# Optimization experiments

Measured on AMD Instinct MI355X. Metric: run time of the kernel, lower is better.

Reference implementation:

```python
import jax, jax.numpy as jnp
import numpy as np

B, H, C = 1, 4, 32
D = H * C          # 128
S, L = 128, 256
EPS = 1e-5


def _axial_layer_norm(x, gamma, beta):
    # normalize over channel axis (axis=1) of [B, D, S, L]
    mu = jnp.mean(x, axis=1, keepdims=True)
    var = jnp.var(x, axis=1, keepdims=True)
    xn = (x - mu) * jax.lax.rsqrt(var + EPS)
    return xn * gamma[None, :, None, None] + beta[None, :, None, None]


def setup_inputs() -> dict:
    key = jax.random.key(0)
    ks = jax.random.split(key, 5)
    x = jax.random.normal(ks[0], (B, D, S, L), dtype=jnp.float32)
    w_row = jax.random.normal(ks[1], (3 * D, D), dtype=jnp.float32) * 0.02
    b_row = jax.random.normal(ks[2], (3 * D,), dtype=jnp.float32) * 0.02
    w_col = jax.random.normal(ks[3], (3 * D, D), dtype=jnp.float32) * 0.02
    b_col = jax.random.normal(ks[4], (3 * D,), dtype=jnp.float32) * 0.02
    return {
        "x": x,
        "w_row": w_row, "b_row": b_row,
        "w_col": w_col, "b_col": b_col,
        "gamma1": jnp.ones((D,), jnp.float32), "beta1": jnp.zeros((D,), jnp.float32),
        "gamma2": jnp.ones((D,), jnp.float32), "beta2": jnp.zeros((D,), jnp.float32),
    }


def _qkv(x, w, b):
    # 1x1 conv == channel matmul: [3D, D] x [B, D, S, L] -> [B, 3D, S, L]
    qkv = jnp.einsum('od,bdsl->bosl', w, x) + b[None, :, None, None]
    q, k, v = jnp.split(qkv, 3, axis=1)
    rs = lambda t: t.reshape(t.shape[0], H, C, S, L)
    return rs(q), rs(k), rs(v)


def reference(x, w_row, b_row, w_col, b_col, gamma1, beta1, gamma2, beta2):
    # --- row attention (attend along L within each row s) ---
    q, k, v = _qkv(x, w_row, b_row)
    row_attn = jnp.einsum('bhcsi,bhcsj->bhsij', q, k)   # [B,H,S,L,L], no 1/sqrt(d) scaling (as in source)
    row_attn = jax.nn.softmax(row_attn, axis=-1)
    row_out = jnp.einsum('bhsij,bhdsj->bhdsi', row_attn, v).reshape(x.shape[0], D, S, L)
    out = _axial_layer_norm(x + row_out, gamma1, beta1)

    # --- column attention (attend along S within each column l) ---
    q, k, v = _qkv(out, w_col, b_col)
    col_attn = jnp.einsum('bhcil,bhcjl->bhijl', q, k)   # [B,H,S,S,L]
    col_attn = jax.nn.softmax(col_attn, axis=-2)
    col_out = jnp.einsum('bhijl,bhdjl->bhdil', col_attn, v).reshape(x.shape[0], D, S, L)
    out = _axial_layer_norm(out + col_out, gamma2, beta2)
    return out
```

## Files before the change

kernel.cpp:

```cpp
#include <hip/hip_runtime.h>
#include <hip/hip_bf16.h>

#define SL     32768
#define EPS_LN 1e-5f

typedef unsigned short u16;
typedef __attribute__((ext_vector_type(8))) short bf16x8;
typedef __attribute__((ext_vector_type(4))) float f32x4;

#define MFMA16(a, b, c) __builtin_amdgcn_mfma_f32_16x16x32_bf16((a), (b), (c), 0, 0, 0)

__device__ inline u16 f2bf(float f) {
    __hip_bfloat16 h = __float2bfloat16(f);
    return *reinterpret_cast<u16*>(&h);
}
__device__ inline float bf2f(u16 u) {
    unsigned v = ((unsigned)u) << 16;
    float f;
    __builtin_memcpy(&f, &v, 4);
    return f;
}
__device__ inline uint4 pack8(float4 a, float4 b) {
    union { uint4 v; u16 u[8]; } U;
    U.u[0] = f2bf(a.x); U.u[1] = f2bf(a.y); U.u[2] = f2bf(a.z); U.u[3] = f2bf(a.w);
    U.u[4] = f2bf(b.x); U.u[5] = f2bf(b.y); U.u[6] = f2bf(b.z); U.u[7] = f2bf(b.w);
    return U.v;
}

__global__ __launch_bounds__(256) void wcast_kernel(const float* __restrict__ wr,
                                                    const float* __restrict__ wc,
                                                    u16* __restrict__ wrb,
                                                    u16* __restrict__ wcb) {
    const int i = blockIdx.x * 256 + threadIdx.x;
    const int NW = 384 * 128 / 8;
    const float* src = (i < NW) ? wr : wc;
    u16* dst = (i < NW) ? wrb : wcb;
    const int j = (i < NW) ? i : i - NW;
    float4 a = ((const float4*)src)[j * 2];
    float4 b = ((const float4*)src)[j * 2 + 1];
    ((uint4*)dst)[j] = pack8(a, b);
}

__global__ __launch_bounds__(512) void qkv_mfma(const float* __restrict__ in,
                                                const u16* __restrict__ wb,
                                                const float* __restrict__ bq,
                                                u16* __restrict__ qT,
                                                u16* __restrict__ kT,
                                                u16* __restrict__ vb) {
    __shared__ u16 xT[64][136];
    __shared__ float bs[384];
    const int n0 = blockIdx.x * 64;
    const int t = threadIdx.x;
    const int lane = t & 63, wv = t >> 6, lo = lane & 15, hi = lane >> 4;

    if (t < 384) bs[t] = bq[t];

    #pragma unroll
    for (int itr = 0; itr < 2; ++itr) {
        const int u = t + itr * 512;
        const int d = u & 127, noct = u >> 7;
        const float* src = in + (size_t)d * SL + n0 + noct * 8;
        float4 f0 = *(const float4*)src;
        float4 f1 = *(const float4*)(src + 4);
        xT[noct * 8 + 0][d] = f2bf(f0.x);
        xT[noct * 8 + 1][d] = f2bf(f0.y);
        xT[noct * 8 + 2][d] = f2bf(f0.z);
        xT[noct * 8 + 3][d] = f2bf(f0.w);
        xT[noct * 8 + 4][d] = f2bf(f1.x);
        xT[noct * 8 + 5][d] = f2bf(f1.y);
        xT[noct * 8 + 6][d] = f2bf(f1.z);
        xT[noct * 8 + 7][d] = f2bf(f1.w);
    }
    __syncthreads();

    bf16x8 af[3][4];
    #pragma unroll
    for (int om = 0; om < 3; ++om)
        #pragma unroll
        for (int ks = 0; ks < 4; ++ks)
            af[om][ks] = *(const bf16x8*)(wb + (size_t)(wv * 48 + om * 16 + lo) * 128
                                             + hi * 8 + ks * 32);

    #pragma unroll
    for (int nt = 0; nt < 4; ++nt) {
        const int n = n0 + nt * 16 + lo;
        bf16x8 bfr[4];
        #pragma unroll
        for (int ks = 0; ks < 4; ++ks)
            bfr[ks] = *(const bf16x8*)&xT[nt * 16 + lo][hi * 8 + ks * 32];
        #pragma unroll
        for (int om = 0; om < 3; ++om) {
            const int obase = wv * 48 + om * 16;
            f32x4 acc = {0.f, 0.f, 0.f, 0.f};
            #pragma unroll
            for (int ks = 0; ks < 4; ++ks)
                acc = MFMA16(af[om][ks], bfr[ks], acc);
            if (obase < 256) {
                u16* tbuf = (obase < 128) ? qT : kT;
                const int ob = obase & 127;
                const int h = ob >> 5;
                const int cb = (ob & 31) + hi * 4;
                ushort4 o4;
                o4.x = f2bf(acc[0] + bs[obase + hi * 4 + 0]);
                o4.y = f2bf(acc[1] + bs[obase + hi * 4 + 1]);
                o4.z = f2bf(acc[2] + bs[obase + hi * 4 + 2]);
                o4.w = f2bf(acc[3] + bs[obase + hi * 4 + 3]);
                *(ushort4*)(tbuf + (size_t)h * SL * 32 + (size_t)n * 32 + cb) = o4;
            } else {
                const int orow = obase - 256 + hi * 4;
                #pragma unroll
                for (int r = 0; r < 4; ++r)
                    vb[(size_t)(orow + r) * SL + n] = f2bf(acc[r] + bs[obase + hi * 4 + r]);
            }
        }
    }
}

template<int KLEN, int NTHR>
__global__ __launch_bounds__(NTHR) void attn_kernel(const u16* __restrict__ qT,
                                                    const u16* __restrict__ kT,
                                                    const u16* __restrict__ vb,
                                                    u16* __restrict__ ao) {
    constexpr int NJT = KLEN / 16;
    constexpr int NW = NTHR / 64;
    constexpr int NOUT = SL / KLEN;
    __shared__ u16 PT[NW][2][16][36];

    const int bid = blockIdx.x;
    const int outer = bid % NOUT;
    const int h = bid / NOUT;
    const int base = outer * KLEN;
    const int t = threadIdx.x;
    const int lane = t & 63, wv = t >> 6, lo = lane & 15, hi = lane >> 4;
    const int i0w = wv * 32;

    const u16* qh = qT + (size_t)h * SL * 32;
    const u16* kh = kT + (size_t)h * SL * 32;
    const u16* vh = vb + (size_t)h * 32 * SL;

    bf16x8 qf0 = *(const bf16x8*)(qh + (size_t)(base + i0w + lo) * 32 + hi * 8);
    bf16x8 qf1 = *(const bf16x8*)(qh + (size_t)(base + i0w + 16 + lo) * 32 + hi * 8);

    f32x4 o00 = {0.f, 0.f, 0.f, 0.f}, o01 = {0.f, 0.f, 0.f, 0.f};
    f32x4 o10 = {0.f, 0.f, 0.f, 0.f}, o11 = {0.f, 0.f, 0.f, 0.f};
    float ls0[4] = {0.f, 0.f, 0.f, 0.f};
    float ls1[4] = {0.f, 0.f, 0.f, 0.f};

    #pragma unroll
    for (int jt = 0; jt < NJT; ++jt) {
        bf16x8 kf = *(const bf16x8*)(kh + (size_t)(base + jt * 16 + lo) * 32 + hi * 8);
        f32x4 z = {0.f, 0.f, 0.f, 0.f};
        f32x4 s0 = MFMA16(qf0, kf, z);
        f32x4 s1 = MFMA16(qf1, kf, z);
        #pragma unroll
        for (int r = 0; r < 4; ++r) {
            float p0 = __expf(s0[r]);
            ls0[r] += p0;
            PT[wv][0][hi * 4 + r][(jt & 1) * 16 + lo] = f2bf(p0);
            float p1 = __expf(s1[r]);
            ls1[r] += p1;
            PT[wv][1][hi * 4 + r][(jt & 1) * 16 + lo] = f2bf(p1);
        }
        if (jt & 1) {
            const int jb = (jt - 1) * 16;
            bf16x8 pf0 = *(const bf16x8*)&PT[wv][0][lo][hi * 8];
            bf16x8 pf1 = *(const bf16x8*)&PT[wv][1][lo][hi * 8];
            bf16x8 v0 = *(const bf16x8*)(vh + (size_t)lo * SL + base + jb + hi * 8);
            bf16x8 v1 = *(const bf16x8*)(vh + (size_t)(16 + lo) * SL + base + jb + hi * 8);
            o00 = MFMA16(pf0, v0, o00);
            o01 = MFMA16(pf0, v1, o01);
            o10 = MFMA16(pf1, v0, o10);
            o11 = MFMA16(pf1, v1, o11);
        }
    }
    #pragma unroll
    for (int r = 0; r < 4; ++r) {
        float v0 = ls0[r];
        v0 += __shfl_xor(v0, 1);
        v0 += __shfl_xor(v0, 2);
        v0 += __shfl_xor(v0, 4);
        v0 += __shfl_xor(v0, 8);
        ls0[r] = 1.f / v0;
        float v1 = ls1[r];
        v1 += __shfl_xor(v1, 1);
        v1 += __shfl_xor(v1, 2);
        v1 += __shfl_xor(v1, 4);
        v1 += __shfl_xor(v1, 8);
        ls1[r] = 1.f / v1;
    }
    {
        ushort4 o4;
        o4.x = f2bf(o00[0] * ls0[0]);
        o4.y = f2bf(o00[1] * ls0[1]);
        o4.z = f2bf(o00[2] * ls0[2]);
        o4.w = f2bf(o00[3] * ls0[3]);
        *(ushort4*)(ao + (size_t)(h * 32 + lo) * SL + base + i0w + hi * 4) = o4;
        o4.x = f2bf(o01[0] * ls0[0]);
        o4.y = f2bf(o01[1] * ls0[1]);
        o4.z = f2bf(o01[2] * ls0[2]);
        o4.w = f2bf(o01[3] * ls0[3]);
        *(ushort4*)(ao + (size_t)(h * 32 + 16 + lo) * SL + base + i0w + hi * 4) = o4;
        o4.x = f2bf(o10[0] * ls1[0]);
        o4.y = f2bf(o10[1] * ls1[1]);
        o4.z = f2bf(o10[2] * ls1[2]);
        o4.w = f2bf(o10[3] * ls1[3]);
        *(ushort4*)(ao + (size_t)(h * 32 + lo) * SL + base + i0w + 16 + hi * 4) = o4;
        o4.x = f2bf(o11[0] * ls1[0]);
        o4.y = f2bf(o11[1] * ls1[1]);
        o4.z = f2bf(o11[2] * ls1[2]);
        o4.w = f2bf(o11[3] * ls1[3]);
        *(ushort4*)(ao + (size_t)(h * 32 + 16 + lo) * SL + base + i0w + 16 + hi * 4) = o4;
    }
}

__global__ __launch_bounds__(512) void qkv_attn2(const u16* __restrict__ in,
                                                 const u16* __restrict__ wb,
                                                 const float* __restrict__ bq,
                                                 u16* __restrict__ ao) {
    __shared__ u16 xS[128][136];
    __shared__ u16 qkS[2][4][128][36];
    __shared__ u16 vS[4][32][136];
    __shared__ u16 PT[8][2][16][36];
    __shared__ float bs[384];

    const int l = blockIdx.x;
    const size_t p0 = (size_t)l * 128;
    const int t = threadIdx.x;
    const int lane = t & 63, wv = t >> 6, lo = lane & 15, hi = lane >> 4;

    if (t < 384) bs[t] = bq[t];
    #pragma unroll
    for (int itr = 0; itr < 4; ++itr) {
        const int u = t + itr * 512;
        const int n = u >> 4, seg = u & 15;
        *(uint4*)&xS[n][seg * 8] = *(const uint4*)(in + (p0 + n) * 128 + seg * 8);
    }
    __syncthreads();

    bf16x8 af[3][4];
    #pragma unroll
    for (int om = 0; om < 3; ++om)
        #pragma unroll
        for (int ks = 0; ks < 4; ++ks)
            af[om][ks] = *(const bf16x8*)(wb + (size_t)(wv * 48 + om * 16 + lo) * 128
                                             + hi * 8 + ks * 32);
    #pragma unroll
    for (int nt = 0; nt < 8; ++nt) {
        const int n = nt * 16 + lo;
        bf16x8 bfr[4];
        #pragma unroll
        for (int ks = 0; ks < 4; ++ks)
            bfr[ks] = *(const bf16x8*)&xS[n][hi * 8 + ks * 32];
        #pragma unroll
        for (int om = 0; om < 3; ++om) {
            const int obase = wv * 48 + om * 16;
            f32x4 acc = {0.f, 0.f, 0.f, 0.f};
            #pragma unroll
            for (int ks = 0; ks < 4; ++ks)
                acc = MFMA16(af[om][ks], bfr[ks], acc);
            if (obase < 256) {
                const int qk = obase >> 7;
                const int ob = obase & 127;
                const int h = ob >> 5;
                const int cb = (ob & 31) + hi * 4;
                ushort4 o4;
                o4.x = f2bf(acc[0] + bs[obase + hi * 4 + 0]);
                o4.y = f2bf(acc[1] + bs[obase + hi * 4 + 1]);
                o4.z = f2bf(acc[2] + bs[obase + hi * 4 + 2]);
                o4.w = f2bf(acc[3] + bs[obase + hi * 4 + 3]);
                *(ushort4*)&qkS[qk][h][n][cb] = o4;
            } else {
                const int vr = obase - 256 + hi * 4;
                #pragma unroll
                for (int r = 0; r < 4; ++r) {
                    const int o = vr + r;
                    vS[o >> 5][o & 31][n] = f2bf(acc[r] + bs[obase + hi * 4 + r]);
                }
            }
        }
    }
    __syncthreads();

    const int h = wv >> 1;
    u16 (*oS2)[136] = xS;

    #pragma unroll
    for (int g = 0; g < 2; ++g) {
        const int ib = (wv & 1) * 64 + g * 32;
        bf16x8 qf0 = *(const bf16x8*)&qkS[0][h][ib + lo][hi * 8];
        bf16x8 qf1 = *(const bf16x8*)&qkS[0][h][ib + 16 + lo][hi * 8];

        f32x4 o00 = {0.f, 0.f, 0.f, 0.f}, o01 = {0.f, 0.f, 0.f, 0.f};
        f32x4 o10 = {0.f, 0.f, 0.f, 0.f}, o11 = {0.f, 0.f, 0.f, 0.f};
        float ls0[4] = {0.f, 0.f, 0.f, 0.f};
        float ls1[4] = {0.f, 0.f, 0.f, 0.f};

        #pragma unroll
        for (int jt = 0; jt < 8; ++jt) {
            bf16x8 kf = *(const bf16x8*)&qkS[1][h][jt * 16 + lo][hi * 8];
            f32x4 z = {0.f, 0.f, 0.f, 0.f};
            f32x4 s0 = MFMA16(qf0, kf, z);
            f32x4 s1 = MFMA16(qf1, kf, z);
            #pragma unroll
            for (int r = 0; r < 4; ++r) {
                float pv0 = __expf(s0[r]);
                ls0[r] += pv0;
                PT[wv][0][hi * 4 + r][(jt & 1) * 16 + lo] = f2bf(pv0);
                float pv1 = __expf(s1[r]);
                ls1[r] += pv1;
                PT[wv][1][hi * 4 + r][(jt & 1) * 16 + lo] = f2bf(pv1);
            }
            if (jt & 1) {
                const int jb = (jt - 1) * 16;
                bf16x8 pf0 = *(const bf16x8*)&PT[wv][0][lo][hi * 8];
                bf16x8 pf1 = *(const bf16x8*)&PT[wv][1][lo][hi * 8];
                bf16x8 v0 = *(const bf16x8*)&vS[h][lo][jb + hi * 8];
                bf16x8 v1 = *(const bf16x8*)&vS[h][16 + lo][jb + hi * 8];
                o00 = MFMA16(pf0, v0, o00);
                o01 = MFMA16(pf0, v1, o01);
                o10 = MFMA16(pf1, v0, o10);
                o11 = MFMA16(pf1, v1, o11);
            }
        }
        #pragma unroll
        for (int r = 0; r < 4; ++r) {
            float v0 = ls0[r];
            v0 += __shfl_xor(v0, 1);
            v0 += __shfl_xor(v0, 2);
            v0 += __shfl_xor(v0, 4);
            v0 += __shfl_xor(v0, 8);
            ls0[r] = 1.f / v0;
            float v1 = ls1[r];
            v1 += __shfl_xor(v1, 1);
            v1 += __shfl_xor(v1, 2);
            v1 += __shfl_xor(v1, 4);
            v1 += __shfl_xor(v1, 8);
            ls1[r] = 1.f / v1;
        }
        #pragma unroll
        for (int r = 0; r < 4; ++r) {
            oS2[ib + hi * 4 + r][h * 32 + lo]           = f2bf(o00[r] * ls0[r]);
            oS2[ib + hi * 4 + r][h * 32 + 16 + lo]      = f2bf(o01[r] * ls0[r]);
            oS2[ib + 16 + hi * 4 + r][h * 32 + lo]      = f2bf(o10[r] * ls1[r]);
            oS2[ib + 16 + hi * 4 + r][h * 32 + 16 + lo] = f2bf(o11[r] * ls1[r]);
        }
    }
    __syncthreads();

    #pragma unroll
    for (int itr = 0; itr < 4; ++itr) {
        const int u = t + itr * 512;
        const int s = u >> 4, seg = u & 15;
        *(uint4*)(ao + (p0 + s) * 128 + seg * 8) = *(const uint4*)&oS2[s][seg * 8];
    }
}

__global__ __launch_bounds__(256) void ln_mid(const float* __restrict__ in0,
                                              const u16* __restrict__ in1,
                                              const float* __restrict__ g,
                                              const float* __restrict__ be,
                                              u16* __restrict__ outp) {
    __shared__ float val[128][69];
    __shared__ float redS[4][72];
    __shared__ float redQ[4][72];
    __shared__ float stat[64][2];
    __shared__ float gs[128], bes[128];
    const int bid = blockIdx.x;
    const int r0 = (bid / 16) * 4;
    const int c0 = (bid % 16) * 16;
    const int t = threadIdx.x;
    const int pos = t & 63, q = t >> 6;
    const size_t gp = (size_t)(r0 + (pos >> 4)) * 256 + c0 + (pos & 15);

    if (t < 128) { gs[t] = g[t]; bes[t] = be[t]; }
    float s = 0.f, ss = 0.f;
    #pragma unroll 4
    for (int dd = 0; dd < 32; ++dd) {
        const int d = q * 32 + dd;
        float v = in0[(size_t)d * SL + gp] + bf2f(in1[(size_t)d * SL + gp]);
        val[d][pos] = v;
        s += v; ss += v * v;
    }
    redS[q][pos] = s;
    redQ[q][pos] = ss;
    __syncthreads();
    if (t < 64) {
        const float S  = redS[0][t] + redS[1][t] + redS[2][t] + redS[3][t];
        const float SS = redQ[0][t] + redQ[1][t] + redQ[2][t] + redQ[3][t];
        const float mean = S * (1.f / 128.f);
        const float var  = SS * (1.f / 128.f) - mean * mean;
        stat[t][0] = mean;
        stat[t][1] = rsqrtf(var + EPS_LN);
    }
    __syncthreads();

    {
        const int pr = pos >> 4, pc = pos & 15;
        const size_t pp = (size_t)(c0 + pc) * 128 + r0 + pr;
        const float mean = stat[pos][0], rstd = stat[pos][1];
        union { uint4 v[4]; u16 u[32]; } O;
        #pragma unroll
        for (int dd = 0; dd < 32; ++dd) {
            const int d = q * 32 + dd;
            O.u[dd] = f2bf((val[d][pos] - mean) * rstd * gs[d] + bes[d]);
        }
        uint4* dst = (uint4*)(outp + pp * 128 + q * 32);
        #pragma unroll
        for (int k = 0; k < 4; ++k) dst[k] = O.v[k];
    }
}

__global__ __launch_bounds__(256) void ln_out(const u16* __restrict__ in0,
                                              const u16* __restrict__ in1,
                                              const float* __restrict__ g,
                                              const float* __restrict__ be,
                                              float* __restrict__ outp) {
    __shared__ float val[128][69];
    __shared__ float redS[4][72];
    __shared__ float redQ[4][72];
    __shared__ float stat[64][2];
    const int bid = blockIdx.x;
    const int r0 = (bid / 8) * 4;
    const int c0 = (bid % 8) * 16;
    const int t = threadIdx.x;
    const int pos = t & 63, q = t >> 6;
    const size_t gp = (size_t)(r0 + (pos >> 4)) * 128 + c0 + (pos & 15);

    float s = 0.f, ss = 0.f;
    {
        union { uint4 v[4]; u16 u[32]; } A, B;
        const uint4* src0 = (const uint4*)(in0 + gp * 128 + q * 32);
        const uint4* src1 = (const uint4*)(in1 + gp * 128 + q * 32);
        #pragma unroll
        for (int k = 0; k < 4; ++k) { A.v[k] = src0[k]; B.v[k] = src1[k]; }
        #pragma unroll 4
        for (int dd = 0; dd < 32; ++dd) {
            const int d = q * 32 + dd;
            float v = bf2f(A.u[dd]) + bf2f(B.u[dd]);
            val[d][pos] = v;
            s += v; ss += v * v;
        }
    }
    redS[q][pos] = s;
    redQ[q][pos] = ss;
    __syncthreads();
    if (t < 64) {
        const float S  = redS[0][t] + redS[1][t] + redS[2][t] + redS[3][t];
        const float SS = redQ[0][t] + redQ[1][t] + redQ[2][t] + redQ[3][t];
        const float mean = S * (1.f / 128.f);
        const float var  = SS * (1.f / 128.f) - mean * mean;
        stat[t][0] = mean;
        stat[t][1] = rsqrtf(var + EPS_LN);
    }
    __syncthreads();

    {
        const int d = t >> 1;
        const int ch = (t & 1) * 8;
        const float gd = g[d], bd = be[d];
        #pragma unroll
        for (int cc = 0; cc < 8; ++cc) {
            const int c = ch + cc;
            float ov[4];
            #pragma unroll
            for (int r = 0; r < 4; ++r) {
                const int p = r * 16 + c;
                ov[r] = (val[d][p] - stat[p][0]) * stat[p][1] * gd + bd;
            }
            float* dst = outp + (size_t)d * SL + (c0 + c) * 256 + r0;
            *(float4*)dst = make_float4(ov[0], ov[1], ov[2], ov[3]);
        }
    }
}

extern "C" void kernel_launch(void* const* d_in, const int* in_sizes, int n_in,
                              void* d_out, int out_size, void* d_ws, size_t ws_size,
                              hipStream_t stream) {
    const float* x     = (const float*)d_in[0];
    const float* w_row = (const float*)d_in[1];
    const float* b_row = (const float*)d_in[2];
    const float* w_col = (const float*)d_in[3];
    const float* b_col = (const float*)d_in[4];
    const float* g1    = (const float*)d_in[5];
    const float* be1   = (const float*)d_in[6];
    const float* g2    = (const float*)d_in[7];
    const float* be2   = (const float*)d_in[8];
    float* out = (float*)d_out;

    char* base = (char*)d_ws;
    u16* qTb = (u16*)base;                        base += (size_t)128 * SL * 2;
    u16* kTb = (u16*)base;                        base += (size_t)128 * SL * 2;
    u16* vbb = (u16*)base;                        base += (size_t)128 * SL * 2;
    u16* ao16 = (u16*)base;                       base += (size_t)128 * SL * 2;
    u16* o1b  = (u16*)base;                       base += (size_t)128 * SL * 2;
    u16* wrb  = (u16*)base;                       base += (size_t)384 * 128 * 2;
    u16* wcb  = (u16*)base;

    wcast_kernel<<<48, 256, 0, stream>>>(w_row, w_col, wrb, wcb);
    qkv_mfma<<<512, 512, 0, stream>>>(x, wrb, b_row, qTb, kTb, vbb);
    attn_kernel<256, 512><<<512, 512, 0, stream>>>(qTb, kTb, vbb, ao16);
    ln_mid<<<512, 256, 0, stream>>>(x, ao16, g1, be1, o1b);
    qkv_attn2<<<256, 512, 0, stream>>>(o1b, wcb, b_col, ao16);
    ln_out<<<512, 256, 0, stream>>>(o1b, ao16, g2, be2, out);
}
```

Measured before the change: 91.54 us.

## Fuse first layer norm into column QKV+attention kernel

Removes the separate ln_mid kernel and computes the residual-add plus first layer norm inside qkv_attn2 for each column, writing the normalized tile straight into shared memory for the QKV matmul. It still writes o1b to global memory for the final layer norm. This saves one launch and the global round-trip read of o1b. In exchange the input loads are strided (stride 256 elements per position) and less coalesced, and shared buffers are aliased, so the second attention output goes to a reused workspace buffer.

```diff
diff --git a/kernel.cpp b/kernel.cpp
--- a/kernel.cpp
+++ b/kernel.cpp
@@ -213,15 +213,20 @@
     }
 }
 
-__global__ __launch_bounds__(512) void qkv_attn2(const u16* __restrict__ in,
+__global__ __launch_bounds__(512) void qkv_attn2(const float* __restrict__ x,
+                                                 const u16* __restrict__ ao1,
                                                  const u16* __restrict__ wb,
                                                  const float* __restrict__ bq,
-                                                 u16* __restrict__ ao) {
+                                                 const float* __restrict__ g1,
+                                                 const float* __restrict__ be1,
+                                                 u16* __restrict__ o1b,
+                                                 u16* __restrict__ ao2) {
     __shared__ u16 xS[128][136];
     __shared__ u16 qkS[2][4][128][36];
     __shared__ u16 vS[4][32][136];
-    __shared__ u16 PT[8][2][16][36];
+    __shared__ u16 PT[8][2][16][34];
     __shared__ float bs[384];
+    __shared__ float gs[128], bes[128];
 
     const int l = blockIdx.x;
     const size_t p0 = (size_t)l * 128;
@@ -229,11 +234,51 @@
     const int lane = t & 63, wv = t >> 6, lo = lane & 15, hi = lane >> 4;
 
     if (t < 384) bs[t] = bq[t];
-    #pragma unroll
-    for (int itr = 0; itr < 4; ++itr) {
-        const int u = t + itr * 512;
-        const int n = u >> 4, seg = u & 15;
-        *(uint4*)&xS[n][seg * 8] = *(const uint4*)(in + (p0 + n) * 128 + seg * 8);
+    if (t >= 384) { gs[t - 384] = g1[t - 384]; bes[t - 384] = be1[t - 384]; }
+
+    float (*valF)[129] = (float (*)[129])&qkS[0][0][0][0];
+    float* red = (float*)&PT[0][0][0][0];
+    float* redS_ = red;
+    float* redQ_ = red + 512;
+    float* stat_ = red + 1024;
+
+    const int s = t & 127, q = t >> 7;
+    const size_t gp = (size_t)s * 256 + l;
+    {
+        float sum = 0.f, ss = 0.f;
+        #pragma unroll 4
+        for (int dd = 0; dd < 32; ++dd) {
+            const int d = q * 32 + dd;
+            float v = x[(size_t)d * SL + gp] + bf2f(ao1[(size_t)d * SL + gp]);
+            valF[s][d] = v;
+            sum += v; ss += v * v;
+        }
+        redS_[q * 128 + s] = sum;
+        redQ_[q * 128 + s] = ss;
+    }
+    __syncthreads();
+    if (t < 128) {
+        const float S  = redS_[t] + redS_[128 + t] + redS_[256 + t] + redS_[384 + t];
+        const float SS = redQ_[t] + redQ_[128 + t] + redQ_[256 + t] + redQ_[384 + t];
+        const float mean = S * (1.f / 128.f);
+        const float var  = SS * (1.f / 128.f) - mean * mean;
+        stat_[t * 2]     = mean;
+        stat_[t * 2 + 1] = rsqrtf(var + EPS_LN);
+    }
+    __syncthreads();
+    {
+        const float mean = stat_[s * 2], rstd = stat_[s * 2 + 1];
+        union { uint4 v[4]; u16 u[32]; } O;
+        #pragma unroll
+        for (int dd = 0; dd < 32; ++dd) {
+            const int d = q * 32 + dd;
+            O.u[dd] = f2bf((valF[s][d] - mean) * rstd * gs[d] + bes[d]);
+        }
+        #pragma unroll
+        for (int k = 0; k < 4; ++k) *(uint4*)&xS[s][q * 32 + k * 8] = O.v[k];
+        uint4* dst = (uint4*)(o1b + (p0 + s) * 128 + q * 32);
+        #pragma unroll
+        for (int k = 0; k < 4; ++k) dst[k] = O.v[k];
     }
     __syncthreads();
 
@@ -350,63 +395,8 @@
     #pragma unroll
     for (int itr = 0; itr < 4; ++itr) {
         const int u = t + itr * 512;
-        const int s = u >> 4, seg = u & 15;
-        *(uint4*)(ao + (p0 + s) * 128 + seg * 8) = *(const uint4*)&oS2[s][seg * 8];
-    }
-}
-
-__global__ __launch_bounds__(256) void ln_mid(const float* __restrict__ in0,
-                                              const u16* __restrict__ in1,
-                                              const float* __restrict__ g,
-                                              const float* __restrict__ be,
-                                              u16* __restrict__ outp) {
-    __shared__ float val[128][69];
-    __shared__ float redS[4][72];
-    __shared__ float redQ[4][72];
-    __shared__ float stat[64][2];
-    __shared__ float gs[128], bes[128];
-    const int bid = blockIdx.x;
-    const int r0 = (bid / 16) * 4;
-    const int c0 = (bid % 16) * 16;
-    const int t = threadIdx.x;
-    const int pos = t & 63, q = t >> 6;
-    const size_t gp = (size_t)(r0 + (pos >> 4)) * 256 + c0 + (pos & 15);
-
-    if (t < 128) { gs[t] = g[t]; bes[t] = be[t]; }
-    float s = 0.f, ss = 0.f;
-    #pragma unroll 4
-    for (int dd = 0; dd < 32; ++dd) {
-        const int d = q * 32 + dd;
-        float v = in0[(size_t)d * SL + gp] + bf2f(in1[(size_t)d * SL + gp]);
-        val[d][pos] = v;
-        s += v; ss += v * v;
-    }
-    redS[q][pos] = s;
-    redQ[q][pos] = ss;
-    __syncthreads();
-    if (t < 64) {
-        const float S  = redS[0][t] + redS[1][t] + redS[2][t] + redS[3][t];
-        const float SS = redQ[0][t] + redQ[1][t] + redQ[2][t] + redQ[3][t];
-        const float mean = S * (1.f / 128.f);
-        const float var  = SS * (1.f / 128.f) - mean * mean;
-        stat[t][0] = mean;
-        stat[t][1] = rsqrtf(var + EPS_LN);
-    }
-    __syncthreads();
-
-    {
-        const int pr = pos >> 4, pc = pos & 15;
-        const size_t pp = (size_t)(c0 + pc) * 128 + r0 + pr;
-        const float mean = stat[pos][0], rstd = stat[pos][1];
-        union { uint4 v[4]; u16 u[32]; } O;
-        #pragma unroll
-        for (int dd = 0; dd < 32; ++dd) {
-            const int d = q * 32 + dd;
-            O.u[dd] = f2bf((val[d][pos] - mean) * rstd * gs[d] + bes[d]);
-        }
-        uint4* dst = (uint4*)(outp + pp * 128 + q * 32);
-        #pragma unroll
-        for (int k = 0; k < 4; ++k) dst[k] = O.v[k];
+        const int sr = u >> 4, seg = u & 15;
+        *(uint4*)(ao2 + (p0 + sr) * 128 + seg * 8) = *(const uint4*)&oS2[sr][seg * 8];
     }
 }
 
@@ -495,11 +485,11 @@
     u16* o1b  = (u16*)base;                       base += (size_t)128 * SL * 2;
     u16* wrb  = (u16*)base;                       base += (size_t)384 * 128 * 2;
     u16* wcb  = (u16*)base;
+    u16* ao2  = qTb;
 
     wcast_kernel<<<48, 256, 0, stream>>>(w_row, w_col, wrb, wcb);
     qkv_mfma<<<512, 512, 0, stream>>>(x, wrb, b_row, qTb, kTb, vbb);
     attn_kernel<256, 512><<<512, 512, 0, stream>>>(qTb, kTb, vbb, ao16);
-    ln_mid<<<512, 256, 0, stream>>>(x, ao16, g1, be1, o1b);
-    qkv_attn2<<<256, 512, 0, stream>>>(o1b, wcb, b_col, ao16);
-    ln_out<<<512, 256, 0, stream>>>(o1b, ao16, g2, be2, out);
-}
+    qkv_attn2<<<256, 512, 0, stream>>>(x, ao16, wcb, b_col, g1, be1, o1b, ao2);
+    ln_out<<<512, 256, 0, stream>>>(o1b, ao2, g2, be2, out);
+}
```

Result: slower. 117.5 us (+28.4%).
